# Optimization experiments

Measured on AMD Instinct MI355X. Metric: run time of the kernel, lower is better.

Reference implementation:

```python
import jax, jax.numpy as jnp
import numpy as np

N_NODES = 16384
N_EDGES = 32768
D = 128          # node feature / hidden dim
EDGE_DIM = 10    # bond featurizer one-hot dim
EH = 32          # edge_hidden_dim in the NNConv MLPs


def _nnconv(x, src, dst, edge_attr, l1w, l1b, l2w, l2b, root, bias):
    """PyG NNConv with aggr='mean': out_i = x_i @ root + mean_{e: dst=i} x_{src_e} @ W(e) + bias."""
    E = edge_attr.shape[0]
    h = jax.nn.relu(edge_attr @ l1w + l1b)              # [E, EH]
    W = (h @ l2w + l2b).reshape(E, D, D)                # per-edge weight matrices [E, D, D]
    msg = jnp.einsum('ei,eio->eo', x[src], W)           # gather + per-edge matmul [E, D]
    s = jax.ops.segment_sum(msg, dst, num_segments=N_NODES)
    cnt = jax.ops.segment_sum(jnp.ones((E, 1), x.dtype), dst, num_segments=N_NODES)
    agg = s / jnp.maximum(cnt, 1.0)                     # scatter-mean (0 for isolated nodes)
    return x @ root + agg + bias


def setup_inputs() -> dict:
    key = jax.random.key(0)
    ks = jax.random.split(key, 14)
    x = jax.random.normal(ks[0], (N_NODES, D), dtype=jnp.float32)
    edge_index = jax.random.randint(ks[1], (2, N_EDGES), 0, N_NODES, dtype=jnp.int64)
    edge_attr = jax.random.uniform(ks[2], (N_EDGES, EDGE_DIM), dtype=jnp.float32)

    def lin(k, fan_in, fan_out):
        return jax.random.normal(k, (fan_in, fan_out), dtype=jnp.float32) / np.sqrt(fan_in)

    return {
        'x': x, 'edge_index': edge_index, 'edge_attr': edge_attr,
        # subgraph_conv1 (128 -> 128)
        'w1_l1': lin(ks[3], EDGE_DIM, EH), 'b1_l1': jnp.zeros((EH,), jnp.float32),
        'w1_l2': lin(ks[4], EH, D * D),    'b1_l2': jnp.zeros((D * D,), jnp.float32),
        'w1_root': lin(ks[5], D, D),       'b1': jnp.zeros((D,), jnp.float32),
        # subgraph_conv2 (128 -> 128), applied twice with shared weights
        'w2_l1': lin(ks[6], EDGE_DIM, EH), 'b2_l1': jnp.zeros((EH,), jnp.float32),
        'w2_l2': lin(ks[7], EH, D * D),    'b2_l2': jnp.zeros((D * D,), jnp.float32),
        'w2_root': lin(ks[8], D, D),       'b2': jnp.zeros((D,), jnp.float32),
    }


def reference(x, edge_index, edge_attr,
              w1_l1, b1_l1, w1_l2, b1_l2, w1_root, b1,
              w2_l1, b2_l1, w2_l2, b2_l2, w2_root, b2):
    src, dst = edge_index[0], edge_index[1]
    h = jax.nn.relu(_nnconv(x, src, dst, edge_attr, w1_l1, b1_l1, w1_l2, b1_l2, w1_root, b1))
    h = jax.nn.relu(_nnconv(h, src, dst, edge_attr, w2_l1, b2_l1, w2_l2, b2_l2, w2_root, b2))
    h = _nnconv(h, src, dst, edge_attr, w2_l1, b2_l1, w2_l2, b2_l2, w2_root, b2)
    return h
```

## Files before the change

### kernel.cpp

```cpp
#include <hip/hip_runtime.h>

#define N_NODES 16384
#define N_EDGES 32768
#define D 128
#define EDGE_DIM 10
#define KH 32
#define BM 64
#define XST2 72
#define XST 136
#define NBL 32

typedef _Float16 f16;
typedef _Float16 f16x4 __attribute__((ext_vector_type(4)));
typedef _Float16 f16x8 __attribute__((ext_vector_type(8)));
typedef float f32x4 __attribute__((ext_vector_type(4)));

__device__ __forceinline__ void ld16(f16x8 &d, const f16* p) {
  asm volatile("global_load_dwordx4 %0, %1, off" : "=v"(d) : "v"(p) : "memory");
}

__global__ __launch_bounds__(256) void deg_pack_kernel(
    const int* __restrict__ ei, int* __restrict__ deg,
    const float* __restrict__ w1l2, const float* __restrict__ w2l2,
    const float* __restrict__ b1l2, const float* __restrict__ b2l2,
    const float* __restrict__ rt1, const float* __restrict__ rt2,
    f16* __restrict__ Bp1, f16* __restrict__ Bp2,
    f16* __restrict__ Rp1, f16* __restrict__ Rp2) {
  int y = blockIdx.y;
  if (y == 0) {
    int e = blockIdx.x * 256 + threadIdx.x;
    if (e < N_EDGES) atomicAdd(&deg[ei[N_EDGES + e]], 1);
    return;
  }
  if (blockIdx.x >= D * D / 256) return;
  int t = blockIdx.x * 256 + threadIdx.x;
  int j = y - 1;
  if (j < 2) {
    const float* l2w = j ? w2l2 : w1l2;
    f16* Bp = j ? Bp2 : Bp1;
    f16 tmp[KH];
#pragma unroll
    for (int k = 0; k < KH; k++) tmp[k] = (f16)l2w[(size_t)k * (D * D) + t];
    f16x8* dst = (f16x8*)(Bp + (size_t)t * KH);
#pragma unroll
    for (int c = 0; c < 4; c++) dst[c] = *(f16x8*)&tmp[c * 8];
  } else {
    const float* src = (j == 2) ? b1l2 : (j == 3) ? b2l2 : (j == 4) ? rt1 : rt2;
    f16* dst = (j == 2) ? (Bp1 + (size_t)D * D * KH)
             : (j == 3) ? (Bp2 + (size_t)D * D * KH)
             : (j == 4) ? Rp1 : Rp2;
    int i = t >> 7, o = t & 127;
    dst[((size_t)(i >> 5) * D + o) * KH + (i & 31)] = (f16)src[t];
  }
}

__global__ __launch_bounds__(1024) void scan_kernel(
    const int* __restrict__ deg, int* __restrict__ rs, int* __restrict__ fill) {
  __shared__ int part[1024];
  int t = threadIdx.x;
  int base = t * 16;
  int loc[16], s = 0;
#pragma unroll
  for (int j = 0; j < 16; j++) { loc[j] = deg[base + j]; s += loc[j]; }
  part[t] = s;
  __syncthreads();
  for (int off = 1; off < 1024; off <<= 1) {
    int add = (t >= off) ? part[t - off] : 0;
    __syncthreads();
    part[t] += add;
    __syncthreads();
  }
  int run = t ? part[t - 1] : 0;
#pragma unroll
  for (int j = 0; j < 16; j++) {
    rs[base + j] = run; fill[base + j] = run; run += loc[j];
  }
  if (t == 1023) rs[N_NODES] = run;
}

__global__ __launch_bounds__(256) void scatter_kernel(
    const int* __restrict__ ei, int* __restrict__ fill,
    int* __restrict__ perm, int* __restrict__ srcs) {
  int e = blockIdx.x * blockDim.x + threadIdx.x;
  if (e < N_EDGES) {
    int pos = atomicAdd(&fill[ei[N_EDGES + e]], 1);
    perm[pos] = e;
    srcs[pos] = ei[e];
  }
}

__global__ __launch_bounds__(256) void edge_mlp_kernel(
    const float* __restrict__ ea, const int* __restrict__ perm,
    const float* __restrict__ w1l1, const float* __restrict__ b1l1,
    const float* __restrict__ w2l1, const float* __restrict__ b2l1,
    f16* __restrict__ h1, f16* __restrict__ h2) {
  int p = blockIdx.x * blockDim.x + threadIdx.x;
  const float* l1w = blockIdx.y ? w2l1 : w1l1;
  const float* l1b = blockIdx.y ? b2l1 : b1l1;
  f16* h = blockIdx.y ? h2 : h1;
  int e = perm[p];
  float a[EDGE_DIM];
#pragma unroll
  for (int d = 0; d < EDGE_DIM; d++) a[d] = ea[e * EDGE_DIM + d];
  f16 hv[KH];
#pragma unroll
  for (int k = 0; k < KH; k++) {
    float acc = l1b[k];
#pragma unroll
    for (int d = 0; d < EDGE_DIM; d++) acc += a[d] * l1w[d * KH + k];
    hv[k] = (f16)fmaxf(acc, 0.0f);
  }
  f16x8* dst = (f16x8*)(h + (size_t)p * KH);
#pragma unroll
  for (int c = 0; c < 4; c++) dst[c] = *(f16x8*)&hv[c * 8];
}

__global__ __launch_bounds__(256, 2) void msg_mfma_kernel(
    const float* __restrict__ xin, const f16* __restrict__ hf,
    const f16* __restrict__ Bp, const int* __restrict__ srcs,
    f16* __restrict__ msgfA, f16* __restrict__ msgfB) {
  __shared__ f16 Xs[BM][XST2];
  __shared__ f16 Hs[BM][KH];
  int t = threadIdx.x;
  int e0 = blockIdx.x * BM;
  int y  = blockIdx.y;
  f16* msgf = y ? msgfB : msgfA;

  ((f16x8*)Hs)[t] = ((const f16x8*)(hf + (size_t)e0 * KH))[t];
  {
    int r = t >> 2, q = t & 3;
    int s = srcs[e0 + r];
    const float4* src = (const float4*)(xin + (size_t)s * D + y * 64 + q * 16);
    f16* dst = &Xs[r][q * 16];
#pragma unroll
    for (int c = 0; c < 4; c++) {
      float4 v = src[c];
      f16x4 h4 = {(f16)v.x, (f16)v.y, (f16)v.z, (f16)v.w};
      *(f16x4*)(dst + c * 4) = h4;
    }
  }

  int L = t & 63, w = t >> 6;
  int quad = L >> 4, lm = L & 15;
  int n0 = w * 32;

  const f16* bl = Bp + ((size_t)(y * 64) * D + n0 + lm) * KH + quad * 8;
  const size_t istr = (size_t)D * KH;

  f32x4 acc[4][2];
#pragma unroll
  for (int mt = 0; mt < 4; mt++)
#pragma unroll
    for (int nt = 0; nt < 2; nt++)
      acc[mt][nt] = (f32x4){0.f, 0.f, 0.f, 0.f};

  f16x8 bufA[4][2], bufB[4][2];

  auto issueB = [&](f16x8 (&buf)[4][2], int basei) {
#pragma unroll
    for (int jj = 0; jj < 4; jj++) {
      const f16* bi = bl + (size_t)(basei + jj) * istr;
      ld16(buf[jj][0], bi);
      ld16(buf[jj][1], bi + 16 * KH);
    }
  };

  auto wait8 = [&]() {
    asm volatile("s_waitcnt vmcnt(8)" ::: "memory");
    __builtin_amdgcn_sched_barrier(0);
  };
  auto wait0 = [&]() {
    asm volatile("s_waitcnt vmcnt(0)" ::: "memory");
    __builtin_amdgcn_sched_barrier(0);
  };

  f16x8 hreg[4];

  auto compute = [&](f16x8 (&buf)[4][2], int ig) {
    f16x4 xv[4];
#pragma unroll
    for (int mt = 0; mt < 4; mt++)
      xv[mt] = *(const f16x4*)&Xs[mt * 16 + lm][ig];
#pragma unroll
    for (int jj = 0; jj < 4; jj++) {
#pragma unroll
      for (int mt = 0; mt < 4; mt++) {
        f16 xs = xv[mt][jj];
        f16x8 xb = {xs, xs, xs, xs, xs, xs, xs, xs};
        f16x8 a = hreg[mt] * xb;
        acc[mt][0] = __builtin_amdgcn_mfma_f32_16x16x32_f16(a, buf[jj][0], acc[mt][0], 0, 0, 0);
        acc[mt][1] = __builtin_amdgcn_mfma_f32_16x16x32_f16(a, buf[jj][1], acc[mt][1], 0, 0, 0);
      }
    }
  };

  __syncthreads();

#pragma unroll
  for (int mt = 0; mt < 4; mt++)
    hreg[mt] = *(const f16x8*)&Hs[mt * 16 + lm][quad * 8];

  issueB(bufA, 0);
  issueB(bufB, 4);

#pragma unroll 1
  for (int gi = 0; gi < 7; gi++) {
    wait8();
    compute(bufA, 8 * gi);
    issueB(bufA, 8 * gi + 8);
    wait8();
    compute(bufB, 8 * gi + 4);
    issueB(bufB, 8 * gi + 12);
  }
  wait8();
  compute(bufA, 56);
  wait0();
  compute(bufB, 60);

  {
    const f16* bb = Bp + (size_t)D * D * KH;
#pragma unroll
    for (int g2 = 0; g2 < 2; g2++) {
      int ig2 = 2 * y + g2;
      const f16* b2l = bb + ((size_t)ig2 * D + n0 + lm) * KH + quad * 8;
      f16x8 b0 = *(const f16x8*)b2l;
      f16x8 b1 = *(const f16x8*)(b2l + 16 * KH);
      int lc = g2 * 32 + quad * 8;
#pragma unroll
      for (int mt = 0; mt < 4; mt++) {
        f16x8 a = *(const f16x8*)&Xs[mt * 16 + lm][lc];
        acc[mt][0] = __builtin_amdgcn_mfma_f32_16x16x32_f16(a, b0, acc[mt][0], 0, 0, 0);
        acc[mt][1] = __builtin_amdgcn_mfma_f32_16x16x32_f16(a, b1, acc[mt][1], 0, 0, 0);
      }
    }
  }

#pragma unroll
  for (int mt = 0; mt < 4; mt++)
#pragma unroll
    for (int r = 0; r < 4; r++) {
      f16* mg = msgf + (size_t)(e0 + mt * 16 + quad * 4 + r) * D + n0 + lm;
      mg[0]  = (f16)acc[mt][0][r];
      mg[16] = (f16)acc[mt][1][r];
    }
}

__global__ __launch_bounds__(256) void node_update_kernel(
    const float* __restrict__ xin, const f16* __restrict__ msgA,
    const f16* __restrict__ msgB, const int* __restrict__ rs,
    const f16* __restrict__ Rp, const float* __restrict__ bias,
    float* __restrict__ out, int do_relu) {
  __shared__ f16 Xs[NBL][XST];
  __shared__ float Sls[NBL][D];
  int t = threadIdx.x;
  int nb = blockIdx.x * NBL;

  {
    int r = t >> 3, q = t & 7;
    const float4* src = (const float4*)(xin + (size_t)(nb + r) * D + q * 16);
    f16* dst = &Xs[r][q * 16];
#pragma unroll
    for (int c = 0; c < 4; c++) {
      float4 v = src[c];
      f16x4 h4 = {(f16)v.x, (f16)v.y, (f16)v.z, (f16)v.w};
      *(f16x4*)(dst + c * 4) = h4;
    }
  }
  __syncthreads();

  {
    int nl = t >> 3, o0 = (t & 7) * 16;
    int n = nb + nl;
    int a = rs[n], b = rs[n + 1];
    float sum[16];
#pragma unroll
    for (int j = 0; j < 16; j++) sum[j] = 0.f;
    for (int r = a; r < b; r++) {
      f16x8 a0 = *(const f16x8*)(msgA + (size_t)r * D + o0);
      f16x8 a1 = *(const f16x8*)(msgA + (size_t)r * D + o0 + 8);
      f16x8 b0 = *(const f16x8*)(msgB + (size_t)r * D + o0);
      f16x8 b1 = *(const f16x8*)(msgB + (size_t)r * D + o0 + 8);
#pragma unroll
      for (int j = 0; j < 8; j++) {
        sum[j]     += (float)a0[j] + (float)b0[j];
        sum[8 + j] += (float)a1[j] + (float)b1[j];
      }
    }
    float inv = 1.0f / (float)max(b - a, 1);
#pragma unroll
    for (int j = 0; j < 16; j++) Sls[nl][o0 + j] = sum[j] * inv;
  }
  __syncthreads();

  int L = t & 63, w = t >> 6;
  int quad = L >> 4, lm = L & 15;
  int n0 = w * 32;
  f32x4 acc[2][2];
#pragma unroll
  for (int mt = 0; mt < 2; mt++)
#pragma unroll
    for (int nt = 0; nt < 2; nt++)
      acc[mt][nt] = (f32x4){0.f, 0.f, 0.f, 0.f};
#pragma unroll
  for (int s4 = 0; s4 < 4; s4++) {
    const f16* b2l = Rp + ((size_t)s4 * D + n0 + lm) * KH + quad * 8;
    f16x8 b0 = *(const f16x8*)b2l;
    f16x8 b1 = *(const f16x8*)(b2l + 16 * KH);
#pragma unroll
    for (int mt = 0; mt < 2; mt++) {
      f16x8 a = *(const f16x8*)&Xs[mt * 16 + lm][s4 * 32 + quad * 8];
      acc[mt][0] = __builtin_amdgcn_mfma_f32_16x16x32_f16(a, b0, acc[mt][0], 0, 0, 0);
      acc[mt][1] = __builtin_amdgcn_mfma_f32_16x16x32_f16(a, b1, acc[mt][1], 0, 0, 0);
    }
  }
#pragma unroll
  for (int mt = 0; mt < 2; mt++)
#pragma unroll
    for (int r = 0; r < 4; r++) {
      Sls[mt * 16 + quad * 4 + r][n0 + lm] += acc[mt][0][r];
      Sls[mt * 16 + quad * 4 + r][n0 + 16 + lm] += acc[mt][1][r];
    }
  __syncthreads();

  {
    int o = t & 127, g = t >> 7;
    float bo = bias[o];
    for (int q = g * 16; q < g * 16 + 16; q++) {
      float v = bo + Sls[q][o];
      out[(size_t)(nb + q) * D + o] = do_relu ? fmaxf(v, 0.0f) : v;
    }
  }
}

extern "C" void kernel_launch(void* const* d_in, const int* in_sizes, int n_in,
                              void* d_out, int out_size, void* d_ws, size_t ws_size,
                              hipStream_t stream) {
  const float* x      = (const float*)d_in[0];
  const int*   ei     = (const int*)d_in[1];
  const float* ea     = (const float*)d_in[2];
  const float* w1_l1  = (const float*)d_in[3];
  const float* b1_l1  = (const float*)d_in[4];
  const float* w1_l2  = (const float*)d_in[5];
  const float* b1_l2  = (const float*)d_in[6];
  const float* w1_rt  = (const float*)d_in[7];
  const float* b1     = (const float*)d_in[8];
  const float* w2_l1  = (const float*)d_in[9];
  const float* b2_l1  = (const float*)d_in[10];
  const float* w2_l2  = (const float*)d_in[11];
  const float* b2_l2  = (const float*)d_in[12];
  const float* w2_rt  = (const float*)d_in[13];
  const float* b2     = (const float*)d_in[14];
  float* out = (float*)d_out;

  const size_t BPSZ = (size_t)D * D * KH + (size_t)D * D + 32768;
  f16* h1f = (f16*)d_ws;
  f16* h2f = h1f + (size_t)N_EDGES * KH;
  f16* Bp1 = h2f + (size_t)N_EDGES * KH;
  f16* Bp2 = Bp1 + BPSZ;
  f16* Rp1 = Bp2 + BPSZ;
  f16* Rp2 = Rp1 + (size_t)D * D;
  int* deg  = (int*)(Rp2 + (size_t)D * D);
  int* rs   = deg + N_NODES;
  int* fill = rs + N_NODES + 128;
  int* perm = fill + N_NODES;
  int* srcs = perm + N_EDGES;
  f16* msgA = (f16*)(srcs + N_EDGES);
  f16* msgB = msgA + (size_t)N_EDGES * D;

  hipMemsetAsync(deg, 0, N_NODES * sizeof(int), stream);
  deg_pack_kernel<<<dim3(N_EDGES / 256, 7), 256, 0, stream>>>(
      ei, deg, w1_l2, w2_l2, b1_l2, b2_l2, w1_rt, w2_rt, Bp1, Bp2, Rp1, Rp2);
  scan_kernel<<<1, 1024, 0, stream>>>(deg, rs, fill);
  scatter_kernel<<<N_EDGES / 256, 256, 0, stream>>>(ei, fill, perm, srcs);
  edge_mlp_kernel<<<dim3(N_EDGES / 256, 2), 256, 0, stream>>>(
      ea, perm, w1_l1, b1_l1, w2_l1, b2_l1, h1f, h2f);

  msg_mfma_kernel<<<dim3(N_EDGES / BM, 2), 256, 0, stream>>>(x, h1f, Bp1, srcs, msgA, msgB);
  node_update_kernel<<<N_NODES / NBL, 256, 0, stream>>>(x, msgA, msgB, rs, Rp1, b1, out, 1);
  msg_mfma_kernel<<<dim3(N_EDGES / BM, 2), 256, 0, stream>>>(out, h2f, Bp2, srcs, msgA, msgB);
  node_update_kernel<<<N_NODES / NBL, 256, 0, stream>>>(out, msgA, msgB, rs, Rp2, b2, out, 1);
  msg_mfma_kernel<<<dim3(N_EDGES / BM, 2), 256, 0, stream>>>(out, h2f, Bp2, srcs, msgA, msgB);
  node_update_kernel<<<N_NODES / NBL, 256, 0, stream>>>(out, msgA, msgB, rs, Rp2, b2, out, 0);
}
```

Before: 257.2 us.

## Fold edge MLP into pack kernel, halve node-update tile, prefetch messages

The edge MLP is now computed in original edge order inside the degree/pack kernel, which removes one launch. The message kernel then gathers hidden rows through perm instead of reading them in sorted order. The node update kernel processes 16 nodes per block instead of 32, which doubles the number of blocks, and it software-prefetches the next message row in the segment loop. MFMA sections in the message kernel are wrapped in s_setprio to favour matrix issue. The trade-offs are an indirect gather for the hidden features and less MFMA work per node-update block.

```diff
diff --git a/kernel.cpp b/kernel.cpp
--- a/kernel.cpp
+++ b/kernel.cpp
@@ -8,7 +8,7 @@
 #define BM 64
 #define XST2 72
 #define XST 136
-#define NBL 32
+#define NBL 16
 
 typedef _Float16 f16;
 typedef _Float16 f16x4 __attribute__((ext_vector_type(4)));
@@ -25,11 +25,36 @@
     const float* __restrict__ b1l2, const float* __restrict__ b2l2,
     const float* __restrict__ rt1, const float* __restrict__ rt2,
     f16* __restrict__ Bp1, f16* __restrict__ Bp2,
-    f16* __restrict__ Rp1, f16* __restrict__ Rp2) {
+    f16* __restrict__ Rp1, f16* __restrict__ Rp2,
+    const float* __restrict__ ea,
+    const float* __restrict__ w1l1, const float* __restrict__ b1l1,
+    const float* __restrict__ w2l1, const float* __restrict__ b2l1,
+    f16* __restrict__ h1, f16* __restrict__ h2) {
   int y = blockIdx.y;
   if (y == 0) {
     int e = blockIdx.x * 256 + threadIdx.x;
     if (e < N_EDGES) atomicAdd(&deg[ei[N_EDGES + e]], 1);
+    return;
+  }
+  if (y >= 7) {
+    int e = blockIdx.x * 256 + threadIdx.x;
+    const float* l1w = (y == 8) ? w2l1 : w1l1;
+    const float* l1b = (y == 8) ? b2l1 : b1l1;
+    f16* h = (y == 8) ? h2 : h1;
+    float a[EDGE_DIM];
+#pragma unroll
+    for (int d = 0; d < EDGE_DIM; d++) a[d] = ea[e * EDGE_DIM + d];
+    f16 hv[KH];
+#pragma unroll
+    for (int k = 0; k < KH; k++) {
+      float acc = l1b[k];
+#pragma unroll
+      for (int d = 0; d < EDGE_DIM; d++) acc += a[d] * l1w[d * KH + k];
+      hv[k] = (f16)fmaxf(acc, 0.0f);
+    }
+    f16x8* dst = (f16x8*)(h + (size_t)e * KH);
+#pragma unroll
+    for (int c = 0; c < 4; c++) dst[c] = *(f16x8*)&hv[c * 8];
     return;
   }
   if (blockIdx.x >= D * D / 256) return;
@@ -89,35 +114,10 @@
   }
 }
 
-__global__ __launch_bounds__(256) void edge_mlp_kernel(
-    const float* __restrict__ ea, const int* __restrict__ perm,
-    const float* __restrict__ w1l1, const float* __restrict__ b1l1,
-    const float* __restrict__ w2l1, const float* __restrict__ b2l1,
-    f16* __restrict__ h1, f16* __restrict__ h2) {
-  int p = blockIdx.x * blockDim.x + threadIdx.x;
-  const float* l1w = blockIdx.y ? w2l1 : w1l1;
-  const float* l1b = blockIdx.y ? b2l1 : b1l1;
-  f16* h = blockIdx.y ? h2 : h1;
-  int e = perm[p];
-  float a[EDGE_DIM];
-#pragma unroll
-  for (int d = 0; d < EDGE_DIM; d++) a[d] = ea[e * EDGE_DIM + d];
-  f16 hv[KH];
-#pragma unroll
-  for (int k = 0; k < KH; k++) {
-    float acc = l1b[k];
-#pragma unroll
-    for (int d = 0; d < EDGE_DIM; d++) acc += a[d] * l1w[d * KH + k];
-    hv[k] = (f16)fmaxf(acc, 0.0f);
-  }
-  f16x8* dst = (f16x8*)(h + (size_t)p * KH);
-#pragma unroll
-  for (int c = 0; c < 4; c++) dst[c] = *(f16x8*)&hv[c * 8];
-}
-
 __global__ __launch_bounds__(256, 2) void msg_mfma_kernel(
     const float* __restrict__ xin, const f16* __restrict__ hf,
     const f16* __restrict__ Bp, const int* __restrict__ srcs,
+    const int* __restrict__ perm,
     f16* __restrict__ msgfA, f16* __restrict__ msgfB) {
   __shared__ f16 Xs[BM][XST2];
   __shared__ f16 Hs[BM][KH];
@@ -126,7 +126,11 @@
   int y  = blockIdx.y;
   f16* msgf = y ? msgfB : msgfA;
 
-  ((f16x8*)Hs)[t] = ((const f16x8*)(hf + (size_t)e0 * KH))[t];
+  {
+    int r4 = t >> 2, q4 = t & 3;
+    int ep = perm[e0 + r4];
+    *(f16x8*)&Hs[r4][q4 * 8] = *(const f16x8*)(hf + (size_t)ep * KH + q4 * 8);
+  }
   {
     int r = t >> 2, q = t & 3;
     int s = srcs[e0 + r];
@@ -181,6 +185,7 @@
 #pragma unroll
     for (int mt = 0; mt < 4; mt++)
       xv[mt] = *(const f16x4*)&Xs[mt * 16 + lm][ig];
+    __builtin_amdgcn_s_setprio(1);
 #pragma unroll
     for (int jj = 0; jj < 4; jj++) {
 #pragma unroll
@@ -192,6 +197,7 @@
         acc[mt][1] = __builtin_amdgcn_mfma_f32_16x16x32_f16(a, buf[jj][1], acc[mt][1], 0, 0, 0);
       }
     }
+    __builtin_amdgcn_s_setprio(0);
   };
 
   __syncthreads();
@@ -256,11 +262,11 @@
   int nb = blockIdx.x * NBL;
 
   {
-    int r = t >> 3, q = t & 7;
-    const float4* src = (const float4*)(xin + (size_t)(nb + r) * D + q * 16);
-    f16* dst = &Xs[r][q * 16];
-#pragma unroll
-    for (int c = 0; c < 4; c++) {
+    int r = t >> 4, q = t & 15;
+    const float4* src = (const float4*)(xin + (size_t)(nb + r) * D + q * 8);
+    f16* dst = &Xs[r][q * 8];
+#pragma unroll
+    for (int c = 0; c < 2; c++) {
       float4 v = src[c];
       f16x4 h4 = {(f16)v.x, (f16)v.y, (f16)v.z, (f16)v.w};
       *(f16x4*)(dst + c * 4) = h4;
@@ -269,63 +275,58 @@
   __syncthreads();
 
   {
-    int nl = t >> 3, o0 = (t & 7) * 16;
+    int nl = t >> 4, o0 = (t & 15) * 8;
     int n = nb + nl;
     int a = rs[n], b = rs[n + 1];
-    float sum[16];
-#pragma unroll
-    for (int j = 0; j < 16; j++) sum[j] = 0.f;
+    float sum[8];
+#pragma unroll
+    for (int j = 0; j < 8; j++) sum[j] = 0.f;
+    f16x8 pa, pb;
+    if (a < b) {
+      pa = *(const f16x8*)(msgA + (size_t)a * D + o0);
+      pb = *(const f16x8*)(msgB + (size_t)a * D + o0);
+    }
     for (int r = a; r < b; r++) {
-      f16x8 a0 = *(const f16x8*)(msgA + (size_t)r * D + o0);
-      f16x8 a1 = *(const f16x8*)(msgA + (size_t)r * D + o0 + 8);
-      f16x8 b0 = *(const f16x8*)(msgB + (size_t)r * D + o0);
-      f16x8 b1 = *(const f16x8*)(msgB + (size_t)r * D + o0 + 8);
-#pragma unroll
-      for (int j = 0; j < 8; j++) {
-        sum[j]     += (float)a0[j] + (float)b0[j];
-        sum[8 + j] += (float)a1[j] + (float)b1[j];
+      f16x8 ca = pa, cb = pb;
+      if (r + 1 < b) {
+        pa = *(const f16x8*)(msgA + (size_t)(r + 1) * D + o0);
+        pb = *(const f16x8*)(msgB + (size_t)(r + 1) * D + o0);
       }
+#pragma unroll
+      for (int j = 0; j < 8; j++) sum[j] += (float)ca[j] + (float)cb[j];
     }
     float inv = 1.0f / (float)max(b - a, 1);
 #pragma unroll
-    for (int j = 0; j < 16; j++) Sls[nl][o0 + j] = sum[j] * inv;
+    for (int j = 0; j < 8; j++) Sls[nl][o0 + j] = sum[j] * inv;
   }
   __syncthreads();
 
   int L = t & 63, w = t >> 6;
   int quad = L >> 4, lm = L & 15;
   int n0 = w * 32;
-  f32x4 acc[2][2];
-#pragma unroll
-  for (int mt = 0; mt < 2; mt++)
-#pragma unroll
-    for (int nt = 0; nt < 2; nt++)
-      acc[mt][nt] = (f32x4){0.f, 0.f, 0.f, 0.f};
+  f32x4 acc[2];
+  acc[0] = (f32x4){0.f, 0.f, 0.f, 0.f};
+  acc[1] = (f32x4){0.f, 0.f, 0.f, 0.f};
 #pragma unroll
   for (int s4 = 0; s4 < 4; s4++) {
     const f16* b2l = Rp + ((size_t)s4 * D + n0 + lm) * KH + quad * 8;
     f16x8 b0 = *(const f16x8*)b2l;
     f16x8 b1 = *(const f16x8*)(b2l + 16 * KH);
-#pragma unroll
-    for (int mt = 0; mt < 2; mt++) {
-      f16x8 a = *(const f16x8*)&Xs[mt * 16 + lm][s4 * 32 + quad * 8];
-      acc[mt][0] = __builtin_amdgcn_mfma_f32_16x16x32_f16(a, b0, acc[mt][0], 0, 0, 0);
-      acc[mt][1] = __builtin_amdgcn_mfma_f32_16x16x32_f16(a, b1, acc[mt][1], 0, 0, 0);
-    }
-  }
-#pragma unroll
-  for (int mt = 0; mt < 2; mt++)
-#pragma unroll
-    for (int r = 0; r < 4; r++) {
-      Sls[mt * 16 + quad * 4 + r][n0 + lm] += acc[mt][0][r];
-      Sls[mt * 16 + quad * 4 + r][n0 + 16 + lm] += acc[mt][1][r];
-    }
+    f16x8 a = *(const f16x8*)&Xs[lm][s4 * 32 + quad * 8];
+    acc[0] = __builtin_amdgcn_mfma_f32_16x16x32_f16(a, b0, acc[0], 0, 0, 0);
+    acc[1] = __builtin_amdgcn_mfma_f32_16x16x32_f16(a, b1, acc[1], 0, 0, 0);
+  }
+#pragma unroll
+  for (int r = 0; r < 4; r++) {
+    Sls[quad * 4 + r][n0 + lm] += acc[0][r];
+    Sls[quad * 4 + r][n0 + 16 + lm] += acc[1][r];
+  }
   __syncthreads();
 
   {
     int o = t & 127, g = t >> 7;
     float bo = bias[o];
-    for (int q = g * 16; q < g * 16 + 16; q++) {
+    for (int q = g * 8; q < g * 8 + 8; q++) {
       float v = bo + Sls[q][o];
       out[(size_t)(nb + q) * D + o] = do_relu ? fmaxf(v, 0.0f) : v;
     }
@@ -368,17 +369,16 @@
   f16* msgB = msgA + (size_t)N_EDGES * D;
 
   hipMemsetAsync(deg, 0, N_NODES * sizeof(int), stream);
-  deg_pack_kernel<<<dim3(N_EDGES / 256, 7), 256, 0, stream>>>(
-      ei, deg, w1_l2, w2_l2, b1_l2, b2_l2, w1_rt, w2_rt, Bp1, Bp2, Rp1, Rp2);
+  deg_pack_kernel<<<dim3(N_EDGES / 256, 9), 256, 0, stream>>>(
+      ei, deg, w1_l2, w2_l2, b1_l2, b2_l2, w1_rt, w2_rt, Bp1, Bp2, Rp1, Rp2,
+      ea, w1_l1, b1_l1, w2_l1, b2_l1, h1f, h2f);
   scan_kernel<<<1, 1024, 0, stream>>>(deg, rs, fill);
   scatter_kernel<<<N_EDGES / 256, 256, 0, stream>>>(ei, fill, perm, srcs);
-  edge_mlp_kernel<<<dim3(N_EDGES / 256, 2), 256, 0, stream>>>(
-      ea, perm, w1_l1, b1_l1, w2_l1, b2_l1, h1f, h2f);
-
-  msg_mfma_kernel<<<dim3(N_EDGES / BM, 2), 256, 0, stream>>>(x, h1f, Bp1, srcs, msgA, msgB);
+
+  msg_mfma_kernel<<<dim3(N_EDGES / BM, 2), 256, 0, stream>>>(x, h1f, Bp1, srcs, perm, msgA, msgB);
   node_update_kernel<<<N_NODES / NBL, 256, 0, stream>>>(x, msgA, msgB, rs, Rp1, b1, out, 1);
-  msg_mfma_kernel<<<dim3(N_EDGES / BM, 2), 256, 0, stream>>>(out, h2f, Bp2, srcs, msgA, msgB);
+  msg_mfma_kernel<<<dim3(N_EDGES / BM, 2), 256, 0, stream>>>(out, h2f, Bp2, srcs, perm, msgA, msgB);
   node_update_kernel<<<N_NODES / NBL, 256, 0, stream>>>(out, msgA, msgB, rs, Rp2, b2, out, 1);
-  msg_mfma_kernel<<<dim3(N_EDGES / BM, 2), 256, 0, stream>>>(out, h2f, Bp2, srcs, msgA, msgB);
+  msg_mfma_kernel<<<dim3(N_EDGES / BM, 2), 256, 0, stream>>>(out, h2f, Bp2, srcs, perm, msgA, msgB);
   node_update_kernel<<<N_NODES / NBL, 256, 0, stream>>>(out, msgA, msgB, rs, Rp2, b2, out, 0);
 }
```

Result: faster. 250.7 us (-2.5%).
